# Performance work log

Hardware: AMD Instinct MI355X
Metric: run time of the kernel (lower is better)

Reference implementation:

```python
import jax, jax.numpy as jnp
import numpy as np

B, L, D = 64, 4096, 1024
FILL = -10000.0  # sentinel used by the original masked_fill before the sort


def setup_inputs() -> dict:
    key = jax.random.key(0)
    k1, k2 = jax.random.split(key)
    features = jax.random.normal(k1, (B, L, D), dtype=jnp.float32)
    lengths = jax.random.randint(k2, (B,), 0, L, dtype=jnp.int32)
    return {"features": features, "lengths": lengths}


def reference(features, lengths):
    # Original: mask invalid positions with -10000, sort descending along seq,
    # zero out masked slots, take element 0. Mathematically this is a masked
    # max over valid positions (and 0 if a sequence has length 0, since the
    # second masked_fill zeroes position 0 when mask[:,0] is False).
    L_ = features.shape[1]
    mask = jnp.arange(L_)[None, :] < lengths[:, None]            # [B, L]
    masked = jnp.where(mask[:, :, None], features, FILL)          # [B, L, D]
    pooled = jnp.max(masked, axis=1)                              # [B, D]
    pooled = jnp.where((lengths > 0)[:, None], pooled, 0.0)
    pool_weights = None
    return pooled
```

## Files before the change

kernel.cpp:

```cpp
#include <hip/hip_runtime.h>

#define FILLV (-10000.0f)

typedef __attribute__((ext_vector_type(4))) float f32x4;

__device__ __forceinline__ f32x4 vmax4(f32x4 a, f32x4 b) {
    f32x4 r;
    r.x = fmaxf(a.x, b.x);
    r.y = fmaxf(a.y, b.y);
    r.z = fmaxf(a.z, b.z);
    r.w = fmaxf(a.w, b.w);
    return r;
}

__device__ __forceinline__ f32x4 ntload(const f32x4* p) {
    return __builtin_nontemporal_load(p);
}

__device__ __forceinline__ f32x4 fillv4() {
    f32x4 v = {FILLV, FILLV, FILLV, FILLV};
    return v;
}

__global__ __launch_bounds__(256, 4)
void feasel_partial_kernel(const float* __restrict__ feat,
                           const int* __restrict__ lengths,
                           float* __restrict__ part,
                           int B, int L, int DV, int seg, int S) {
    __shared__ int off[1025];
    const int t = threadIdx.x;

    for (int b = t; b < B; b += blockDim.x) {
        int len = lengths[b];
        len = len < 0 ? 0 : (len > L ? L : len);
        int n = (len + seg - 1) / seg;
        if (n > S) n = S;
        off[b + 1] = n;
    }
    __syncthreads();
    if (t == 0) {
        off[0] = 0;
        for (int b = 0; b < B; ++b) off[b + 1] += off[b];
    }
    __syncthreads();
    const int W = off[B];

    for (int i = blockIdx.x; i < W; i += gridDim.x) {
        int lo = 0, hi = B;
        while (hi - lo > 1) {
            int m = (lo + hi) >> 1;
            if (off[m] <= i) lo = m; else hi = m;
        }
        const int b = lo;
        const int s = i - off[lo];

        int len = lengths[b];
        len = len > L ? L : len;
        const int l0 = s * seg;
        const int l1 = min(l0 + seg, len);

        const f32x4* __restrict__ p =
            reinterpret_cast<const f32x4*>(feat) + (size_t)b * L * DV + (size_t)l0 * DV + t;

        f32x4 a0 = fillv4(), a1 = fillv4(), a2 = fillv4(), a3 = fillv4();
        f32x4 a4 = fillv4(), a5 = fillv4(), a6 = fillv4(), a7 = fillv4();

        int l = l0;
        for (; l + 16 <= l1; l += 16) {
            f32x4 v0  = ntload(p +  0 * (size_t)DV);
            f32x4 v1  = ntload(p +  1 * (size_t)DV);
            f32x4 v2  = ntload(p +  2 * (size_t)DV);
            f32x4 v3  = ntload(p +  3 * (size_t)DV);
            f32x4 v4  = ntload(p +  4 * (size_t)DV);
            f32x4 v5  = ntload(p +  5 * (size_t)DV);
            f32x4 v6  = ntload(p +  6 * (size_t)DV);
            f32x4 v7  = ntload(p +  7 * (size_t)DV);
            f32x4 v8  = ntload(p +  8 * (size_t)DV);
            f32x4 v9  = ntload(p +  9 * (size_t)DV);
            f32x4 v10 = ntload(p + 10 * (size_t)DV);
            f32x4 v11 = ntload(p + 11 * (size_t)DV);
            f32x4 v12 = ntload(p + 12 * (size_t)DV);
            f32x4 v13 = ntload(p + 13 * (size_t)DV);
            f32x4 v14 = ntload(p + 14 * (size_t)DV);
            f32x4 v15 = ntload(p + 15 * (size_t)DV);
            a0 = vmax4(a0, vmax4(v0,  v8));
            a1 = vmax4(a1, vmax4(v1,  v9));
            a2 = vmax4(a2, vmax4(v2,  v10));
            a3 = vmax4(a3, vmax4(v3,  v11));
            a4 = vmax4(a4, vmax4(v4,  v12));
            a5 = vmax4(a5, vmax4(v5,  v13));
            a6 = vmax4(a6, vmax4(v6,  v14));
            a7 = vmax4(a7, vmax4(v7,  v15));
            p += 16 * (size_t)DV;
        }
        for (; l + 4 <= l1; l += 4) {
            a0 = vmax4(a0, ntload(p + 0 * (size_t)DV));
            a1 = vmax4(a1, ntload(p + 1 * (size_t)DV));
            a2 = vmax4(a2, ntload(p + 2 * (size_t)DV));
            a3 = vmax4(a3, ntload(p + 3 * (size_t)DV));
            p += 4 * (size_t)DV;
        }
        for (; l < l1; ++l) {
            a0 = vmax4(a0, ntload(p));
            p += DV;
        }
        a0 = vmax4(a0, a1);
        a2 = vmax4(a2, a3);
        a4 = vmax4(a4, a5);
        a6 = vmax4(a6, a7);
        a0 = vmax4(vmax4(a0, a2), vmax4(a4, a6));

        reinterpret_cast<f32x4*>(part)[((size_t)b * S + s) * DV + t] = a0;
    }
}

__global__ void feasel_reduce_kernel(const float* __restrict__ part,
                                     const int* __restrict__ lengths,
                                     float* __restrict__ out,
                                     int L, int DV, int seg, int S) {
    const int b = blockIdx.x;
    const int c = blockIdx.y * 64 + threadIdx.x;
    if (c >= DV) return;

    int len = lengths[b];
    len = len < 0 ? 0 : (len > L ? L : len);
    int nseg = (len + seg - 1) / seg;
    if (nseg > S) nseg = S;

    f32x4 acc;
    if (len <= 0) {
        f32x4 z = {0.f, 0.f, 0.f, 0.f};
        acc = z;
    } else {
        const f32x4* __restrict__ p =
            reinterpret_cast<const f32x4*>(part) + (size_t)b * S * DV + c;
        f32x4 a0 = fillv4(), a1 = fillv4(), a2 = fillv4(), a3 = fillv4();
        int s = 0;
        for (; s + 4 <= nseg; s += 4) {
            a0 = vmax4(a0, p[(size_t)(s + 0) * DV]);
            a1 = vmax4(a1, p[(size_t)(s + 1) * DV]);
            a2 = vmax4(a2, p[(size_t)(s + 2) * DV]);
            a3 = vmax4(a3, p[(size_t)(s + 3) * DV]);
        }
        for (; s < nseg; ++s)
            a0 = vmax4(a0, p[(size_t)s * DV]);
        acc = vmax4(vmax4(a0, a1), vmax4(a2, a3));
    }
    reinterpret_cast<f32x4*>(out)[(size_t)b * DV + c] = acc;
}

__global__ void feasel_direct_kernel(const float* __restrict__ feat,
                                     const int* __restrict__ lengths,
                                     float* __restrict__ out,
                                     int L, int DV) {
    const int b = blockIdx.x;
    const int t = threadIdx.x;
    int len = lengths[b];
    len = len < 0 ? 0 : (len > L ? L : len);

    const f32x4* __restrict__ p =
        reinterpret_cast<const f32x4*>(feat) + (size_t)b * L * DV + t;

    f32x4 a0 = fillv4(), a1 = fillv4(), a2 = fillv4(), a3 = fillv4();
    int l = 0;
    for (; l + 4 <= len; l += 4) {
        a0 = vmax4(a0, ntload(p + 0 * (size_t)DV));
        a1 = vmax4(a1, ntload(p + 1 * (size_t)DV));
        a2 = vmax4(a2, ntload(p + 2 * (size_t)DV));
        a3 = vmax4(a3, ntload(p + 3 * (size_t)DV));
        p += 4 * (size_t)DV;
    }
    for (; l < len; ++l) {
        a0 = vmax4(a0, ntload(p));
        p += DV;
    }
    a0 = vmax4(vmax4(a0, a1), vmax4(a2, a3));
    if (len <= 0) {
        f32x4 z = {0.f, 0.f, 0.f, 0.f};
        a0 = z;
    }
    reinterpret_cast<f32x4*>(out)[(size_t)b * DV + t] = a0;
}

extern "C" void kernel_launch(void* const* d_in, const int* in_sizes, int n_in,
                              void* d_out, int out_size, void* d_ws, size_t ws_size,
                              hipStream_t stream) {
    const float* feat    = (const float*)d_in[0];
    const int*   lengths = (const int*)d_in[1];
    float*       out     = (float*)d_out;

    const int B  = in_sizes[1];
    const int D  = out_size / B;
    const int DV = D / 4;
    const int L  = in_sizes[0] / (B * D);

    int S = 128;
    while (S > 1 && (size_t)B * S * D * sizeof(float) > ws_size) S >>= 1;

    if ((size_t)B * S * D * sizeof(float) <= ws_size && B <= 1024) {
        float* part   = (float*)d_ws;
        const int seg = (L + S - 1) / S;

        feasel_partial_kernel<<<1024, 256, 0, stream>>>(feat, lengths, part,
                                                        B, L, DV, seg, S);

        dim3 grid2(B, (DV + 63) / 64);
        feasel_reduce_kernel<<<grid2, 64, 0, stream>>>(part, lengths, out, L, DV, seg, S);
    } else {
        feasel_direct_kernel<<<B, DV, 0, stream>>>(feat, lengths, out, L, DV);
    }
}
```

Baseline: 102.7 us.

## Balance work by splitting total valid rows evenly across a fixed grid of blocks

Replaces the fixed per-sequence segment decomposition with a flat partition of all valid rows across exactly G=1024 blocks. Each block scans a contiguous range of valid rows that may span sequence boundaries and writes one partial per sequence it touches. The reduce kernel recomputes the same prefix sums and mapping to combine those partials. The aim is to remove load imbalance from variable lengths and ragged last segments. In exchange, every block runs a serial prefix sum over B on a single thread, and there is extra index arithmetic.

```diff
diff --git a/kernel.cpp b/kernel.cpp
--- a/kernel.cpp
+++ b/kernel.cpp
@@ -22,51 +22,72 @@
     return v;
 }
 
+
 __global__ __launch_bounds__(256, 4)
-void feasel_partial_kernel(const float* __restrict__ feat,
-                           const int* __restrict__ lengths,
-                           float* __restrict__ part,
-                           int B, int L, int DV, int seg, int S) {
-    __shared__ int off[1025];
+void feasel_rows_partial_kernel(const float* __restrict__ feat,
+                                const int* __restrict__ lengths,
+                                float* __restrict__ part,
+                                int B, int L, int DV, int G) {
+    __shared__ int rowstart[1025];
+    __shared__ int slotbase[1025];
     const int t = threadIdx.x;
+    const int j = blockIdx.x;
+
+    if (t == 0) {
+        rowstart[0] = 0;
+        for (int b = 0; b < B; ++b) {
+            int len = lengths[b];
+            len = len < 0 ? 0 : (len > L ? L : len);
+            rowstart[b + 1] = rowstart[b] + len;
+        }
+    }
+    __syncthreads();
+    const int W = rowstart[B];
 
     for (int b = t; b < B; b += blockDim.x) {
-        int len = lengths[b];
-        len = len < 0 ? 0 : (len > L ? L : len);
-        int n = (len + seg - 1) / seg;
-        if (n > S) n = S;
-        off[b + 1] = n;
-    }
-    __syncthreads();
-    if (t == 0) {
-        off[0] = 0;
-        for (int b = 0; b < B; ++b) off[b + 1] += off[b];
-    }
-    __syncthreads();
-    const int W = off[B];
-
-    for (int i = blockIdx.x; i < W; i += gridDim.x) {
-        int lo = 0, hi = B;
-        while (hi - lo > 1) {
-            int m = (lo + hi) >> 1;
-            if (off[m] <= i) lo = m; else hi = m;
-        }
-        const int b = lo;
-        const int s = i - off[lo];
-
-        int len = lengths[b];
-        len = len > L ? L : len;
-        const int l0 = s * seg;
-        const int l1 = min(l0 + seg, len);
+        int s = 0;
+        if (W > 0 && rowstart[b + 1] > rowstart[b]) {
+            int jlo = (int)((unsigned long long)rowstart[b] * G / W);
+            int jhi = (int)((unsigned long long)(rowstart[b + 1] - 1) * G / W);
+            s = jhi - jlo + 1;
+        }
+        slotbase[b + 1] = s;
+    }
+    __syncthreads();
+    if (t == 0) {
+        slotbase[0] = 0;
+        for (int b = 0; b < B; ++b) slotbase[b + 1] += slotbase[b];
+    }
+    __syncthreads();
+
+    if (W == 0) return;
+    const int r0 = (int)(((unsigned long long)W * j + G - 1) / G);
+    int       r1 = (int)(((unsigned long long)W * (j + 1) + G - 1) / G);
+    if (r1 > W) r1 = W;
+    if (r0 >= r1) return;
+
+    int lo = 0, hi = B;
+    while (hi - lo > 1) {
+        int m = (lo + hi) >> 1;
+        if (rowstart[m] <= r0) lo = m; else hi = m;
+    }
+    int b = lo;
+    int r = r0;
+
+    while (r < r1) {
+        while (rowstart[b + 1] <= r) ++b;
+        const int rend  = min(r1, rowstart[b + 1]);
+        const int nrows = rend - r;
+        const int l     = r - rowstart[b];
 
         const f32x4* __restrict__ p =
-            reinterpret_cast<const f32x4*>(feat) + (size_t)b * L * DV + (size_t)l0 * DV + t;
+            reinterpret_cast<const f32x4*>(feat) + ((size_t)b * L + l) * DV + t;
 
         f32x4 a0 = fillv4(), a1 = fillv4(), a2 = fillv4(), a3 = fillv4();
         f32x4 a4 = fillv4(), a5 = fillv4(), a6 = fillv4(), a7 = fillv4();
 
-        int l = l0;
-        for (; l + 16 <= l1; l += 16) {
+        int k = 0;
+        for (; k + 16 <= nrows; k += 16) {
             f32x4 v0  = ntload(p +  0 * (size_t)DV);
             f32x4 v1  = ntload(p +  1 * (size_t)DV);
             f32x4 v2  = ntload(p +  2 * (size_t)DV);
@@ -93,14 +114,14 @@
             a7 = vmax4(a7, vmax4(v7,  v15));
             p += 16 * (size_t)DV;
         }
-        for (; l + 4 <= l1; l += 4) {
+        for (; k + 4 <= nrows; k += 4) {
             a0 = vmax4(a0, ntload(p + 0 * (size_t)DV));
             a1 = vmax4(a1, ntload(p + 1 * (size_t)DV));
             a2 = vmax4(a2, ntload(p + 2 * (size_t)DV));
             a3 = vmax4(a3, ntload(p + 3 * (size_t)DV));
             p += 4 * (size_t)DV;
         }
-        for (; l < l1; ++l) {
+        for (; k < nrows; ++k) {
             a0 = vmax4(a0, ntload(p));
             p += DV;
         }
@@ -110,41 +131,73 @@
         a6 = vmax4(a6, a7);
         a0 = vmax4(vmax4(a0, a2), vmax4(a4, a6));
 
-        reinterpret_cast<f32x4*>(part)[((size_t)b * S + s) * DV + t] = a0;
-    }
-}
-
-__global__ void feasel_reduce_kernel(const float* __restrict__ part,
-                                     const int* __restrict__ lengths,
-                                     float* __restrict__ out,
-                                     int L, int DV, int seg, int S) {
+        const int jlo  = (int)((unsigned long long)rowstart[b] * G / W);
+        const int slot = slotbase[b] + (j - jlo);
+        reinterpret_cast<f32x4*>(part)[(size_t)slot * DV + t] = a0;
+
+        r = rend;
+    }
+}
+
+__global__ void feasel_rows_reduce_kernel(const float* __restrict__ part,
+                                          const int* __restrict__ lengths,
+                                          float* __restrict__ out,
+                                          int B, int L, int DV, int G) {
+    __shared__ int rowstart[1025];
+    __shared__ int slotbase[1025];
+    const int t = threadIdx.x;
+
+    if (t == 0) {
+        rowstart[0] = 0;
+        for (int bb = 0; bb < B; ++bb) {
+            int len = lengths[bb];
+            len = len < 0 ? 0 : (len > L ? L : len);
+            rowstart[bb + 1] = rowstart[bb] + len;
+        }
+    }
+    __syncthreads();
+    const int W = rowstart[B];
+    for (int bb = t; bb < B; bb += blockDim.x) {
+        int s = 0;
+        if (W > 0 && rowstart[bb + 1] > rowstart[bb]) {
+            int jlo = (int)((unsigned long long)rowstart[bb] * G / W);
+            int jhi = (int)((unsigned long long)(rowstart[bb + 1] - 1) * G / W);
+            s = jhi - jlo + 1;
+        }
+        slotbase[bb + 1] = s;
+    }
+    __syncthreads();
+    if (t == 0) {
+        slotbase[0] = 0;
+        for (int bb = 0; bb < B; ++bb) slotbase[bb + 1] += slotbase[bb];
+    }
+    __syncthreads();
+
     const int b = blockIdx.x;
-    const int c = blockIdx.y * 64 + threadIdx.x;
+    const int c = blockIdx.y * 64 + t;
     if (c >= DV) return;
 
-    int len = lengths[b];
-    len = len < 0 ? 0 : (len > L ? L : len);
-    int nseg = (len + seg - 1) / seg;
-    if (nseg > S) nseg = S;
-
+    const int rb0 = rowstart[b], rb1 = rowstart[b + 1];
     f32x4 acc;
-    if (len <= 0) {
+    if (rb1 <= rb0) {
         f32x4 z = {0.f, 0.f, 0.f, 0.f};
         acc = z;
     } else {
-        const f32x4* __restrict__ p =
-            reinterpret_cast<const f32x4*>(part) + (size_t)b * S * DV + c;
-        f32x4 a0 = fillv4(), a1 = fillv4(), a2 = fillv4(), a3 = fillv4();
-        int s = 0;
-        for (; s + 4 <= nseg; s += 4) {
-            a0 = vmax4(a0, p[(size_t)(s + 0) * DV]);
-            a1 = vmax4(a1, p[(size_t)(s + 1) * DV]);
-            a2 = vmax4(a2, p[(size_t)(s + 2) * DV]);
-            a3 = vmax4(a3, p[(size_t)(s + 3) * DV]);
-        }
-        for (; s < nseg; ++s)
-            a0 = vmax4(a0, p[(size_t)s * DV]);
-        acc = vmax4(vmax4(a0, a1), vmax4(a2, a3));
+        const int jlo = (int)((unsigned long long)rb0 * G / W);
+        const int jhi = (int)((unsigned long long)(rb1 - 1) * G / W);
+        acc = fillv4();
+        for (int j = jlo; j <= jhi; ++j) {
+            int br0 = (int)(((unsigned long long)W * j + G - 1) / G);
+            int br1 = (int)(((unsigned long long)W * (j + 1) + G - 1) / G);
+            if (br1 > W) br1 = W;
+            const int is = br0 > rb0 ? br0 : rb0;
+            const int ie = br1 < rb1 ? br1 : rb1;
+            if (is < ie) {
+                const int slot = slotbase[b] + (j - jlo);
+                acc = vmax4(acc,
+                    reinterpret_cast<const f32x4*>(part)[(size_t)slot * DV + c]);
+            }
+        }
     }
     reinterpret_cast<f32x4*>(out)[(size_t)b * DV + c] = acc;
 }
@@ -193,19 +246,19 @@
     const int D  = out_size / B;
     const int DV = D / 4;
     const int L  = in_sizes[0] / (B * D);
-
-    int S = 128;
-    while (S > 1 && (size_t)B * S * D * sizeof(float) > ws_size) S >>= 1;
-
-    if ((size_t)B * S * D * sizeof(float) <= ws_size && B <= 1024) {
-        float* part   = (float*)d_ws;
-        const int seg = (L + S - 1) / S;
-
-        feasel_partial_kernel<<<1024, 256, 0, stream>>>(feat, lengths, part,
-                                                        B, L, DV, seg, S);
+    const int G  = 1024;
+
+    const size_t part_bytes = (size_t)(G + B) * D * sizeof(float);
+
+    if (part_bytes <= ws_size && B <= 1024) {
+        float* part = (float*)d_ws;
+
+        feasel_rows_partial_kernel<<<G, 256, 0, stream>>>(feat, lengths, part,
+                                                          B, L, DV, G);
 
         dim3 grid2(B, (DV + 63) / 64);
-        feasel_reduce_kernel<<<grid2, 64, 0, stream>>>(part, lengths, out, L, DV, seg, S);
+        feasel_rows_reduce_kernel<<<grid2, 64, 0, stream>>>(part, lengths, out,
+                                                            B, L, DV, G);
     } else {
         feasel_direct_kernel<<<B, DV, 0, stream>>>(feat, lengths, out, L, DV);
     }
```

Result: faster. 100.1 us, median of 2 (-2.5%).
